# Kernel tuning notes

Hardware: AMD Instinct MI355X
Metric: run time of the kernel (lower is better)

The kernel has to match this reference:

```python
import jax, jax.numpy as jnp
import numpy as np

E = 128        # embed_dim
D = 384        # d_model
H = 12         # nhead
HD = D // H    # head_dim = 32
E2 = 64        # embed_dim_2d
E1 = 64        # embed_dim_1d
FF = 512       # dim_feedforward
EPS = 1e-5
SCALE = 1.0 / np.sqrt(D)  # dp_attn_norm='d_model'


def layer_norm(x, g, b):
    m = jnp.mean(x, axis=-1, keepdims=True)
    v = jnp.mean(jnp.square(x - m), axis=-1, keepdims=True)
    return (x - m) * jax.lax.rsqrt(v + EPS) * g + b


def setup_inputs() -> dict:
    key = jax.random.key(0)
    ks = jax.random.split(key, 16)
    L, B = 512, 8
    std = 0.02
    return {
        "s": jax.random.normal(ks[0], (L, B, E), jnp.float32),
        "x": jax.random.normal(ks[1], (L, B, E1), jnp.float32),
        "p": jax.random.normal(ks[2], (B, L, L, E2), jnp.float32),
        "Wq": jax.random.normal(ks[3], (E, D), jnp.float32) * std,
        "Wk": jax.random.normal(ks[4], (E, D), jnp.float32) * std,
        "Wv": jax.random.normal(ks[5], (E, D), jnp.float32) * std,
        "Wo": jax.random.normal(ks[6], (D, E), jnp.float32) * std,
        "bo": jnp.zeros((E,), jnp.float32),
        "W2d": jax.random.normal(ks[7], (E2, H), jnp.float32) * std,
        "b2d": jnp.zeros((H,), jnp.float32),
        "W1": jax.random.normal(ks[8], (E + E1, FF), jnp.float32) * std,
        "b1": jnp.zeros((FF,), jnp.float32),
        "W2": jax.random.normal(ks[9], (FF, E), jnp.float32) * std,
        "b2": jnp.zeros((E,), jnp.float32),
        "g1": jnp.ones((E,), jnp.float32),
        "beta1": jnp.zeros((E,), jnp.float32),
        "g2": jnp.ones((E,), jnp.float32),
        "beta2": jnp.zeros((E,), jnp.float32),
    }


def reference(s, x, p, Wq, Wk, Wv, Wo, bo, W2d, b2d, W1, b1, W2, b2,
              g1, beta1, g2, beta2):
    L, B, _ = s.shape
    # --- attention with additive 2D pair bias ---
    # (L,B,E)@(E,D) -> (L,B,D) -> (B,H,L,HD); head split matches torch view(L, B*H, HD)
    def heads(t):
        return jnp.transpose(t.reshape(L, B, H, HD), (1, 2, 0, 3))
    q = heads(s @ Wq) * SCALE
    k = heads(s @ Wk)
    v = heads(s @ Wv)
    scores = jnp.einsum('bhid,bhjd->bhij', q, k)
    pbias = jnp.transpose(p @ W2d + b2d, (0, 3, 1, 2))  # (B,L,L,H) -> (B,H,L,L)
    attn = jax.nn.softmax(scores + pbias, axis=-1)
    o = jnp.einsum('bhij,bhjd->bhid', attn, v)           # (B,H,L,HD)
    o = jnp.transpose(o, (2, 0, 1, 3)).reshape(L, B, D)  # back to (L,B,D)
    s2 = o @ Wo + bo
    # --- residual + post-LN ---
    s = layer_norm(s + s2, g1, beta1)
    # --- FFN on [s, x] concat ---
    um_in = jnp.concatenate([s, x], axis=-1)             # (L,B,E+E1)
    h = jax.nn.relu(um_in @ W1 + b1)
    s2 = h @ W2 + b2
    return layer_norm(s + s2, g2, beta2)
```

## Files before the change

kernel.cpp:

```cpp
#include <hip/hip_runtime.h>
#include <cstdint>
#include <cstddef>

#define EPS 1e-5f

__device__ __forceinline__ float4 ld4(const float* p) { return *(const float4*)p; }
__device__ __forceinline__ void st4(float* p, float4 v) { *(float4*)p = v; }

template<bool RELU>
__launch_bounds__(256)
__global__ void gemm_bias_kernel(const float* __restrict__ A1,
                                 const float* __restrict__ A2, int K1,
                                 const float* __restrict__ W,
                                 const float* __restrict__ bias,
                                 float* __restrict__ out,
                                 int N, int K) {
    __shared__ float As[32 * 68];
    __shared__ float Bs[32 * 68];
    const int tid = threadIdx.x;
    const int bx = blockIdx.x, by = blockIdx.y;
    const int tx = tid & 15, ty = tid >> 4;

    float acc[4][4];
#pragma unroll
    for (int a = 0; a < 4; ++a)
#pragma unroll
        for (int b = 0; b < 4; ++b) acc[a][b] = 0.f;

    for (int k0 = 0; k0 < K; k0 += 32) {
        __syncthreads();
#pragma unroll
        for (int itr = 0; itr < 2; ++itr) {
            int idx = tid + itr * 256;
            int r = idx >> 3, c4 = idx & 7;
            int kk = k0 + c4 * 4;
            const float* src; int rl, kl;
            if (kk < K1) { src = A1; rl = K1; kl = kk; }
            else         { src = A2; rl = K - K1; kl = kk - K1; }
            float4 a = ld4(&src[(size_t)(bx * 64 + r) * rl + kl]);
            As[(c4 * 4 + 0) * 68 + r] = a.x;
            As[(c4 * 4 + 1) * 68 + r] = a.y;
            As[(c4 * 4 + 2) * 68 + r] = a.z;
            As[(c4 * 4 + 3) * 68 + r] = a.w;
            int kb = idx >> 4, n4 = (idx & 15) * 4;
            float4 bvv = ld4(&W[(size_t)(k0 + kb) * N + by * 64 + n4]);
            st4(&Bs[kb * 68 + n4], bvv);
        }
        __syncthreads();
#pragma unroll
        for (int kk2 = 0; kk2 < 32; ++kk2) {
            float4 av = ld4(&As[kk2 * 68 + ty * 4]);
            float4 bv = ld4(&Bs[kk2 * 68 + tx * 4]);
            acc[0][0] = fmaf(av.x, bv.x, acc[0][0]);
            acc[0][1] = fmaf(av.x, bv.y, acc[0][1]);
            acc[0][2] = fmaf(av.x, bv.z, acc[0][2]);
            acc[0][3] = fmaf(av.x, bv.w, acc[0][3]);
            acc[1][0] = fmaf(av.y, bv.x, acc[1][0]);
            acc[1][1] = fmaf(av.y, bv.y, acc[1][1]);
            acc[1][2] = fmaf(av.y, bv.z, acc[1][2]);
            acc[1][3] = fmaf(av.y, bv.w, acc[1][3]);
            acc[2][0] = fmaf(av.z, bv.x, acc[2][0]);
            acc[2][1] = fmaf(av.z, bv.y, acc[2][1]);
            acc[2][2] = fmaf(av.z, bv.z, acc[2][2]);
            acc[2][3] = fmaf(av.z, bv.w, acc[2][3]);
            acc[3][0] = fmaf(av.w, bv.x, acc[3][0]);
            acc[3][1] = fmaf(av.w, bv.y, acc[3][1]);
            acc[3][2] = fmaf(av.w, bv.z, acc[3][2]);
            acc[3][3] = fmaf(av.w, bv.w, acc[3][3]);
        }
    }
    float4 bb = {0.f, 0.f, 0.f, 0.f};
    if (bias) bb = ld4(&bias[by * 64 + tx * 4]);
#pragma unroll
    for (int mi = 0; mi < 4; ++mi) {
        float4 y;
        y.x = acc[mi][0] + bb.x;
        y.y = acc[mi][1] + bb.y;
        y.z = acc[mi][2] + bb.z;
        y.w = acc[mi][3] + bb.w;
        if (RELU) {
            y.x = fmaxf(y.x, 0.f); y.y = fmaxf(y.y, 0.f);
            y.z = fmaxf(y.z, 0.f); y.w = fmaxf(y.w, 0.f);
        }
        st4(&out[(size_t)(bx * 64 + ty * 4 + mi) * N + by * 64 + tx * 4], y);
    }
}

__launch_bounds__(256)
__global__ void attn_kernel(const float* __restrict__ q,
                            const float* __restrict__ k,
                            const float* __restrict__ v,
                            const float* __restrict__ p,
                            const float* __restrict__ w2d,
                            const float* __restrict__ b2d,
                            float* __restrict__ o) {
    __shared__ float q_s[8 * 388];
    __shared__ float k_s[16 * 388];
    __shared__ float v_s[16 * 388];
    __shared__ float e_s[128 * 13];
    __shared__ float l_s[8][12];

    const int tid = threadIdx.x;
    const int it = blockIdx.x;
    const int b  = blockIdx.y;
    const int i0 = it * 8;
    const float scale = 0.05103103630798288f;

    for (int idx = tid; idx < 8 * 96; idx += 256) {
        int r = idx / 96, c4 = (idx % 96) * 4;
        float4 t = ld4(&q[(size_t)((i0 + r) * 8 + b) * 384 + c4]);
        t.x *= scale; t.y *= scale; t.z *= scale; t.w *= scale;
        st4(&q_s[r * 388 + c4], t);
    }

    const int half = __builtin_amdgcn_readfirstlane((int)(tid >> 7));
    const int pair = tid & 127;
    const int pi = pair >> 4, pj = pair & 15;
    const int e0 = half * 32;
    const int d0 = half * 16;
    const int i_b = tid >> 5, l32 = tid & 31;
    const float* w2dh = w2d + e0 * 12;

    float l_part[12];
#pragma unroll
    for (int h = 0; h < 12; ++h) l_part[h] = 0.f;
    float4 oacc[3];
#pragma unroll
    for (int c = 0; c < 3; ++c) { oacc[c].x = 0.f; oacc[c].y = 0.f; oacc[c].z = 0.f; oacc[c].w = 0.f; }

    for (int t = 0; t < 32; ++t) {
        const int j0 = t * 16;
        __syncthreads();
        for (int idx = tid; idx < 16 * 96; idx += 256) {
            int r = idx / 96, c4 = (idx % 96) * 4;
            size_t grow = (size_t)((j0 + r) * 8 + b) * 384 + c4;
            st4(&k_s[r * 388 + c4], ld4(&k[grow]));
            st4(&v_s[r * 388 + c4], ld4(&v[grow]));
        }
        __syncthreads();

        const float* pp = p + (((size_t)b * 512 + (i0 + pi)) * 512 + (j0 + pj)) * 64 + e0;
        float4 pr[8];
#pragma unroll
        for (int c = 0; c < 8; ++c) pr[c] = ld4(pp + c * 4);
        float S[12];
#pragma unroll
        for (int h = 0; h < 12; ++h) S[h] = (half == 0) ? b2d[h] : 0.f;
        const float* prf = (const float*)pr;
#pragma unroll
        for (int e = 0; e < 32; ++e) {
            float pe = prf[e];
#pragma unroll
            for (int h = 0; h < 12; ++h) S[h] = fmaf(pe, w2dh[e * 12 + h], S[h]);
        }
#pragma unroll
        for (int h = 0; h < 12; ++h) {
            const float4* qr4 = (const float4*)&q_s[pi * 388 + h * 32 + d0];
            const float4* kr4 = (const float4*)&k_s[pj * 388 + h * 32 + d0];
            float a0 = 0.f;
#pragma unroll
            for (int dd = 0; dd < 4; ++dd) {
                float4 qa = qr4[dd], ka = kr4[dd];
                a0 = fmaf(qa.x, ka.x, a0); a0 = fmaf(qa.y, ka.y, a0);
                a0 = fmaf(qa.z, ka.z, a0); a0 = fmaf(qa.w, ka.w, a0);
            }
            S[h] += a0;
        }
        if (half == 0) {
#pragma unroll
            for (int h = 0; h < 12; ++h) e_s[pair * 13 + h] = S[h];
        }
        __syncthreads();
        if (half == 1) {
#pragma unroll
            for (int h = 0; h < 12; ++h) {
                float E = __expf(S[h] + e_s[pair * 13 + h]);
                e_s[pair * 13 + h] = E;
                l_part[h] += E;
            }
        }
        __syncthreads();

#pragma unroll
        for (int j = 0; j < 16; ++j) {
            const float* er = &e_s[(i_b * 16 + j) * 13];
#pragma unroll
            for (int c = 0; c < 3; ++c) {
                float prob = er[c * 4 + (l32 >> 3)];
                float4 v4 = ld4(&v_s[j * 388 + c * 128 + l32 * 4]);
                oacc[c].x = fmaf(prob, v4.x, oacc[c].x);
                oacc[c].y = fmaf(prob, v4.y, oacc[c].y);
                oacc[c].z = fmaf(prob, v4.z, oacc[c].z);
                oacc[c].w = fmaf(prob, v4.w, oacc[c].w);
            }
        }
    }

    if (half == 1) {
#pragma unroll
        for (int h = 0; h < 12; ++h) {
            float s0 = l_part[h];
            s0 += __shfl_xor(s0, 1);
            s0 += __shfl_xor(s0, 2);
            s0 += __shfl_xor(s0, 4);
            s0 += __shfl_xor(s0, 8);
            l_part[h] = s0;
        }
        int lane = tid & 63;
        int il = lane >> 4;
        int hh = lane & 15;
        int grp = (tid >> 6) & 1;
        int ig = grp * 4 + il;
#pragma unroll
        for (int h = 0; h < 12; ++h)
            if (hh == h) l_s[ig][h] = l_part[h];
    }
    __syncthreads();
#pragma unroll
    for (int c = 0; c < 3; ++c) {
        float inv = 1.0f / l_s[i_b][c * 4 + (l32 >> 3)];
        float4 y;
        y.x = oacc[c].x * inv; y.y = oacc[c].y * inv;
        y.z = oacc[c].z * inv; y.w = oacc[c].w * inv;
        st4(&o[(size_t)((i0 + i_b) * 8 + b) * 384 + c * 128 + l32 * 4], y);
    }
}

__launch_bounds__(256)
__global__ void ln_kernel(const float* __restrict__ resid,
                          const float* __restrict__ y,
                          const float* __restrict__ g,
                          const float* __restrict__ be,
                          float* __restrict__ out) {
    const int tid = threadIdx.x;
    const int row = blockIdx.x * 2 + (tid >> 7);
    const int c = tid & 127;
    __shared__ float red[4][2];
    size_t idx = (size_t)row * 128 + c;
    float val = resid[idx] + y[idx];
    float s0 = val, sq = val * val;
#pragma unroll
    for (int m = 1; m <= 32; m <<= 1) {
        s0 += __shfl_xor(s0, m);
        sq += __shfl_xor(sq, m);
    }
    const int w = tid >> 6;
    if ((tid & 63) == 0) { red[w][0] = s0; red[w][1] = sq; }
    __syncthreads();
    float S  = red[w][0] + red[w ^ 1][0];
    float SQ = red[w][1] + red[w ^ 1][1];
    float mean = S * (1.f / 128.f);
    float var  = SQ * (1.f / 128.f) - mean * mean;
    out[idx] = (val - mean) * rsqrtf(var + EPS) * g[c] + be[c];
}

extern "C" void kernel_launch(void* const* d_in, const int* in_sizes, int n_in,
                              void* d_out, int out_size, void* d_ws, size_t ws_size,
                              hipStream_t stream) {
    const float* s   = (const float*)d_in[0];
    const float* x   = (const float*)d_in[1];
    const float* p   = (const float*)d_in[2];
    const float* Wq  = (const float*)d_in[3];
    const float* Wk  = (const float*)d_in[4];
    const float* Wv  = (const float*)d_in[5];
    const float* Wo  = (const float*)d_in[6];
    const float* bo  = (const float*)d_in[7];
    const float* W2d = (const float*)d_in[8];
    const float* b2d = (const float*)d_in[9];
    const float* W1  = (const float*)d_in[10];
    const float* b1  = (const float*)d_in[11];
    const float* W2  = (const float*)d_in[12];
    const float* b2  = (const float*)d_in[13];
    const float* g1  = (const float*)d_in[14];
    const float* be1 = (const float*)d_in[15];
    const float* g2  = (const float*)d_in[16];
    const float* be2 = (const float*)d_in[17];
    float* out = (float*)d_out;

    float* ws   = (float*)d_ws;
    float* q_ws = ws;
    float* k_ws = q_ws + 4096 * 384;
    float* v_ws = k_ws + 4096 * 384;
    float* o_ws = v_ws + 4096 * 384;
    float* t1   = o_ws + 4096 * 384;
    float* s1   = t1 + 4096 * 128;
    float* h_ws = s1 + 4096 * 128;
    float* t2   = h_ws + 4096 * 512;

    dim3 blk(256);
    gemm_bias_kernel<false><<<dim3(64, 6), blk, 0, stream>>>(s, nullptr, 128, Wq, nullptr, q_ws, 384, 128);
    gemm_bias_kernel<false><<<dim3(64, 6), blk, 0, stream>>>(s, nullptr, 128, Wk, nullptr, k_ws, 384, 128);
    gemm_bias_kernel<false><<<dim3(64, 6), blk, 0, stream>>>(s, nullptr, 128, Wv, nullptr, v_ws, 384, 128);
    attn_kernel<<<dim3(64, 8), blk, 0, stream>>>(q_ws, k_ws, v_ws, p, W2d, b2d, o_ws);
    gemm_bias_kernel<false><<<dim3(64, 2), blk, 0, stream>>>(o_ws, nullptr, 384, Wo, bo, t1, 128, 384);
    ln_kernel<<<dim3(2048), blk, 0, stream>>>(s, t1, g1, be1, s1);
    gemm_bias_kernel<true ><<<dim3(64, 8), blk, 0, stream>>>(s1, x, 128, W1, b1, h_ws, 512, 192);
    gemm_bias_kernel<false><<<dim3(64, 2), blk, 0, stream>>>(h_ws, nullptr, 512, W2, b2, t2, 128, 512);
    ln_kernel<<<dim3(2048), blk, 0, stream>>>(s1, t2, g2, be2, out);
}
```

Before: 1.048 ms.

## Split attention into MFMA scores and PV kernels with fp16 intermediates

Replaces the monolithic fp32 attention kernel with a scores kernel that computes the pair bias and QK^T via fp16 MFMA and writes exp'd scores to a full fp16 score matrix, plus a separate PV kernel using MFMA that normalizes by row sums. The QKV projections are fused into one launch that emits fp16 with the scale folded in, and the output-projection and FFN2 GEMMs are fused with residual add and LayerNorm. This removes scalar-FMA attention work and several launches, at the cost of writing and re-reading a large score buffer, reduced precision, and no max-subtraction in the softmax.

```diff
diff --git a/kernel.cpp b/kernel.cpp
--- a/kernel.cpp
+++ b/kernel.cpp
@@ -4,8 +4,273 @@
 
 #define EPS 1e-5f
 
+typedef _Float16 f16;
+typedef __attribute__((ext_vector_type(8))) _Float16 f16x8;
+typedef __attribute__((ext_vector_type(4))) _Float16 f16x4;
+typedef __attribute__((ext_vector_type(4))) float f32x4;
+
 __device__ __forceinline__ float4 ld4(const float* p) { return *(const float4*)p; }
 __device__ __forceinline__ void st4(float* p, float4 v) { *(float4*)p = v; }
+
+__launch_bounds__(256)
+__global__ void qkv_kernel(const float* __restrict__ A,
+                           const float* __restrict__ Wq,
+                           const float* __restrict__ Wk,
+                           const float* __restrict__ Wv,
+                           f16* __restrict__ qo, f16* __restrict__ ko,
+                           f16* __restrict__ vo) {
+    __shared__ float As[32 * 68];
+    __shared__ float Bs[32 * 68];
+    const int tid = threadIdx.x;
+    const int bx = blockIdx.x, by = blockIdx.y, z = blockIdx.z;
+    const float* Wp = (z == 0) ? Wq : ((z == 1) ? Wk : Wv);
+    f16* outp = (z == 0) ? qo : ((z == 1) ? ko : vo);
+    const float alpha = (z == 0) ? 0.05103103630798288f : 1.0f;
+    const int tx = tid & 15, ty = tid >> 4;
+    float acc[4][4] = {};
+    for (int k0 = 0; k0 < 128; k0 += 32) {
+        __syncthreads();
+#pragma unroll
+        for (int itr = 0; itr < 2; ++itr) {
+            int idx = tid + itr * 256;
+            int r = idx >> 3, c4 = idx & 7;
+            float4 a = ld4(&A[(size_t)(bx * 64 + r) * 128 + k0 + c4 * 4]);
+            As[(c4 * 4 + 0) * 68 + r] = a.x;
+            As[(c4 * 4 + 1) * 68 + r] = a.y;
+            As[(c4 * 4 + 2) * 68 + r] = a.z;
+            As[(c4 * 4 + 3) * 68 + r] = a.w;
+            int kb = idx >> 4, n4 = (idx & 15) * 4;
+            st4(&Bs[kb * 68 + n4], ld4(&Wp[(size_t)(k0 + kb) * 384 + by * 64 + n4]));
+        }
+        __syncthreads();
+#pragma unroll
+        for (int kk = 0; kk < 32; ++kk) {
+            float4 av = ld4(&As[kk * 68 + ty * 4]);
+            float4 bv = ld4(&Bs[kk * 68 + tx * 4]);
+            acc[0][0] = fmaf(av.x, bv.x, acc[0][0]);
+            acc[0][1] = fmaf(av.x, bv.y, acc[0][1]);
+            acc[0][2] = fmaf(av.x, bv.z, acc[0][2]);
+            acc[0][3] = fmaf(av.x, bv.w, acc[0][3]);
+            acc[1][0] = fmaf(av.y, bv.x, acc[1][0]);
+            acc[1][1] = fmaf(av.y, bv.y, acc[1][1]);
+            acc[1][2] = fmaf(av.y, bv.z, acc[1][2]);
+            acc[1][3] = fmaf(av.y, bv.w, acc[1][3]);
+            acc[2][0] = fmaf(av.z, bv.x, acc[2][0]);
+            acc[2][1] = fmaf(av.z, bv.y, acc[2][1]);
+            acc[2][2] = fmaf(av.z, bv.z, acc[2][2]);
+            acc[2][3] = fmaf(av.z, bv.w, acc[2][3]);
+            acc[3][0] = fmaf(av.w, bv.x, acc[3][0]);
+            acc[3][1] = fmaf(av.w, bv.y, acc[3][1]);
+            acc[3][2] = fmaf(av.w, bv.z, acc[3][2]);
+            acc[3][3] = fmaf(av.w, bv.w, acc[3][3]);
+        }
+    }
+#pragma unroll
+    for (int mi = 0; mi < 4; ++mi) {
+        f16x4 hv;
+        hv[0] = (f16)(acc[mi][0] * alpha);
+        hv[1] = (f16)(acc[mi][1] * alpha);
+        hv[2] = (f16)(acc[mi][2] * alpha);
+        hv[3] = (f16)(acc[mi][3] * alpha);
+        *(f16x4*)&outp[(size_t)(bx * 64 + ty * 4 + mi) * 384 + by * 64 + tx * 4] = hv;
+    }
+}
+
+__launch_bounds__(256)
+__global__ void scores_kernel(const f16* __restrict__ qw,
+                              const f16* __restrict__ kw,
+                              const float* __restrict__ p,
+                              const float* __restrict__ w2d,
+                              const float* __restrict__ b2d,
+                              f16* __restrict__ E) {
+    const int tid = threadIdx.x;
+    const int wv = tid >> 6, lane = tid & 63;
+    const int g = lane >> 4, lj = lane & 15;
+    const int jc = blockIdx.x, it = blockIdx.y, b = blockIdx.z;
+    const int i0 = it * 16, j0 = jc * 64 + wv * 16;
+
+    f16x8 qf[12];
+#pragma unroll
+    for (int h = 0; h < 12; ++h)
+        qf[h] = *(const f16x8*)&qw[((size_t)(i0 + lj) * 8 + b) * 384 + h * 32 + g * 8];
+
+    f32x4 acc[12];
+#pragma unroll
+    for (int h = 0; h < 12; ++h) {
+        float bb = b2d[h];
+        acc[h][0] = bb; acc[h][1] = bb; acc[h][2] = bb; acc[h][3] = bb;
+    }
+
+#pragma unroll
+    for (int r = 0; r < 4; ++r) {
+        const float* prow = p + (((size_t)b * 512 + i0 + g * 4 + r) * 512 + j0 + lj) * 64;
+#pragma unroll
+        for (int hf = 0; hf < 2; ++hf) {
+            float4 pb[8];
+#pragma unroll
+            for (int c = 0; c < 8; ++c) pb[c] = ld4(prow + hf * 32 + c * 4);
+            const float* pf = (const float*)pb;
+#pragma unroll
+            for (int e = 0; e < 32; ++e) {
+                float pe = pf[e];
+                const float* wrow = &w2d[(hf * 32 + e) * 12];
+#pragma unroll
+                for (int h = 0; h < 12; ++h) acc[h][r] = fmaf(pe, wrow[h], acc[h][r]);
+            }
+        }
+    }
+
+    f16x8 kf = *(const f16x8*)&kw[((size_t)(j0 + lj) * 8 + b) * 384 + g * 8];
+#pragma unroll
+    for (int h = 0; h < 12; ++h) {
+        f16x8 kn = kf;
+        if (h < 11)
+            kn = *(const f16x8*)&kw[((size_t)(j0 + lj) * 8 + b) * 384 + (h + 1) * 32 + g * 8];
+        acc[h] = __builtin_amdgcn_mfma_f32_16x16x32_f16(qf[h], kf, acc[h], 0, 0, 0);
+        kf = kn;
+    }
+
+#pragma unroll
+    for (int h = 0; h < 12; ++h) {
+        size_t ebase = (size_t)(b * 12 + h) * 512;
+#pragma unroll
+        for (int r = 0; r < 4; ++r) {
+            E[(ebase + i0 + g * 4 + r) * 512 + j0 + lj] = (f16)__expf(acc[h][r]);
+        }
+    }
+}
+
+__launch_bounds__(256)
+__global__ void pv_kernel(const f16* __restrict__ E,
+                          const f16* __restrict__ vw,
+                          float* __restrict__ o) {
+    __shared__ f16 vt[32][520];
+    const int tid = threadIdx.x;
+    const int bh = blockIdx.x;
+    const int b = bh / 12, h = bh % 12;
+    const int wv = tid >> 6, lane = tid & 63;
+    const int g = lane >> 4, lj = lane & 15;
+    const int i0 = blockIdx.y * 64 + wv * 16;
+
+#pragma unroll
+    for (int itr = 0; itr < 8; ++itr) {
+        int jl = itr * 64 + (tid >> 2);
+        int dc = (tid & 3) * 8;
+        f16x8 sv = *(const f16x8*)&vw[((size_t)jl * 8 + b) * 384 + h * 32 + dc];
+#pragma unroll
+        for (int dd = 0; dd < 8; ++dd) vt[dc + dd][jl] = sv[dd];
+    }
+    __syncthreads();
+
+    f32x4 acc0 = {}, acc1 = {};
+    float lsum = 0.f;
+    const f16* Erow = &E[((size_t)bh * 512 + i0 + lj) * 512];
+#pragma unroll
+    for (int ks = 0; ks < 16; ++ks) {
+        f16x8 af = *(const f16x8*)&Erow[ks * 32 + g * 8];
+        f16x8 b0 = *(const f16x8*)&vt[lj][ks * 32 + g * 8];
+        f16x8 b1 = *(const f16x8*)&vt[16 + lj][ks * 32 + g * 8];
+        acc0 = __builtin_amdgcn_mfma_f32_16x16x32_f16(af, b0, acc0, 0, 0, 0);
+        acc1 = __builtin_amdgcn_mfma_f32_16x16x32_f16(af, b1, acc1, 0, 0, 0);
+#pragma unroll
+        for (int d = 0; d < 8; ++d) lsum += (float)af[d];
+    }
+    lsum += __shfl_xor(lsum, 16);
+    lsum += __shfl_xor(lsum, 32);
+
+#pragma unroll
+    for (int r = 0; r < 4; ++r) {
+        float lr = __shfl(lsum, g * 4 + r);
+        float inv = 1.0f / lr;
+        size_t orow = ((size_t)(i0 + g * 4 + r) * 8 + b) * 384 + h * 32;
+        o[orow + lj] = acc0[r] * inv;
+        o[orow + 16 + lj] = acc1[r] * inv;
+    }
+}
+
+__launch_bounds__(256)
+__global__ void gemm_ln_kernel(const float* __restrict__ A, int K,
+                               const float* __restrict__ Wm,
+                               const float* __restrict__ bias,
+                               const float* __restrict__ resid,
+                               const float* __restrict__ gam,
+                               const float* __restrict__ bet,
+                               float* __restrict__ out) {
+    __shared__ float As[32][36];
+    __shared__ float Bs[32][132];
+    const int tid = threadIdx.x;
+    const int bx = blockIdx.x;
+    const int tx = tid & 31, ty = tid >> 5;
+    float acc[4][4] = {};
+    for (int k0 = 0; k0 < K; k0 += 32) {
+        __syncthreads();
+        {
+            int r = tid >> 3, c4 = tid & 7;
+            float4 a = ld4(&A[(size_t)(bx * 32 + r) * K + k0 + c4 * 4]);
+            As[c4 * 4 + 0][r] = a.x;
+            As[c4 * 4 + 1][r] = a.y;
+            As[c4 * 4 + 2][r] = a.z;
+            As[c4 * 4 + 3][r] = a.w;
+#pragma unroll
+            for (int itr = 0; itr < 4; ++itr) {
+                int idx = tid + itr * 256;
+                int kb = idx >> 5, n4 = (idx & 31) * 4;
+                st4(&Bs[kb][n4], ld4(&Wm[(size_t)(k0 + kb) * 128 + n4]));
+            }
+        }
+        __syncthreads();
+#pragma unroll
+        for (int kk = 0; kk < 32; ++kk) {
+            float4 av = ld4(&As[kk][ty * 4]);
+            float4 bv = ld4(&Bs[kk][tx * 4]);
+            acc[0][0] = fmaf(av.x, bv.x, acc[0][0]);
+            acc[0][1] = fmaf(av.x, bv.y, acc[0][1]);
+            acc[0][2] = fmaf(av.x, bv.z, acc[0][2]);
+            acc[0][3] = fmaf(av.x, bv.w, acc[0][3]);
+            acc[1][0] = fmaf(av.y, bv.x, acc[1][0]);
+            acc[1][1] = fmaf(av.y, bv.y, acc[1][1]);
+            acc[1][2] = fmaf(av.y, bv.z, acc[1][2]);
+            acc[1][3] = fmaf(av.y, bv.w, acc[1][3]);
+            acc[2][0] = fmaf(av.z, bv.x, acc[2][0]);
+            acc[2][1] = fmaf(av.z, bv.y, acc[2][1]);
+            acc[2][2] = fmaf(av.z, bv.z, acc[2][2]);
+            acc[2][3] = fmaf(av.z, bv.w, acc[2][3]);
+            acc[3][0] = fmaf(av.w, bv.x, acc[3][0]);
+            acc[3][1] = fmaf(av.w, bv.y, acc[3][1]);
+            acc[3][2] = fmaf(av.w, bv.z, acc[3][2]);
+            acc[3][3] = fmaf(av.w, bv.w, acc[3][3]);
+        }
+    }
+    float4 bb = ld4(&bias[tx * 4]);
+    float4 gg = ld4(&gam[tx * 4]);
+    float4 be4 = ld4(&bet[tx * 4]);
+#pragma unroll
+    for (int mi = 0; mi < 4; ++mi) {
+        int row = bx * 32 + ty * 4 + mi;
+        float4 r4 = ld4(&resid[(size_t)row * 128 + tx * 4]);
+        float4 y;
+        y.x = acc[mi][0] + bb.x + r4.x;
+        y.y = acc[mi][1] + bb.y + r4.y;
+        y.z = acc[mi][2] + bb.z + r4.z;
+        y.w = acc[mi][3] + bb.w + r4.w;
+        float s = y.x + y.y + y.z + y.w;
+        float sq = y.x * y.x + y.y * y.y + y.z * y.z + y.w * y.w;
+#pragma unroll
+        for (int m = 1; m <= 16; m <<= 1) {
+            s += __shfl_xor(s, m);
+            sq += __shfl_xor(sq, m);
+        }
+        float mean = s * (1.f / 128.f);
+        float var = sq * (1.f / 128.f) - mean * mean;
+        float rs = rsqrtf(var + EPS);
+        float4 w;
+        w.x = (y.x - mean) * rs * gg.x + be4.x;
+        w.y = (y.y - mean) * rs * gg.y + be4.y;
+        w.z = (y.z - mean) * rs * gg.z + be4.z;
+        w.w = (y.w - mean) * rs * gg.w + be4.w;
+        st4(&out[(size_t)row * 128 + tx * 4], w);
+    }
+}
 
 template<bool RELU>
 __launch_bounds__(256)
@@ -20,13 +285,7 @@
     const int tid = threadIdx.x;
     const int bx = blockIdx.x, by = blockIdx.y;
     const int tx = tid & 15, ty = tid >> 4;
-
-    float acc[4][4];
-#pragma unroll
-    for (int a = 0; a < 4; ++a)
-#pragma unroll
-        for (int b = 0; b < 4; ++b) acc[a][b] = 0.f;
-
+    float acc[4][4] = {};
     for (int k0 = 0; k0 < K; k0 += 32) {
         __syncthreads();
 #pragma unroll
@@ -43,8 +302,7 @@
             As[(c4 * 4 + 2) * 68 + r] = a.z;
             As[(c4 * 4 + 3) * 68 + r] = a.w;
             int kb = idx >> 4, n4 = (idx & 15) * 4;
-            float4 bvv = ld4(&W[(size_t)(k0 + kb) * N + by * 64 + n4]);
-            st4(&Bs[kb * 68 + n4], bvv);
+            st4(&Bs[kb * 68 + n4], ld4(&W[(size_t)(k0 + kb) * N + by * 64 + n4]));
         }
         __syncthreads();
 #pragma unroll
@@ -84,174 +342,6 @@
         }
         st4(&out[(size_t)(bx * 64 + ty * 4 + mi) * N + by * 64 + tx * 4], y);
     }
-}
-
-__launch_bounds__(256)
-__global__ void attn_kernel(const float* __restrict__ q,
-                            const float* __restrict__ k,
-                            const float* __restrict__ v,
-                            const float* __restrict__ p,
-                            const float* __restrict__ w2d,
-                            const float* __restrict__ b2d,
-                            float* __restrict__ o) {
-    __shared__ float q_s[8 * 388];
-    __shared__ float k_s[16 * 388];
-    __shared__ float v_s[16 * 388];
-    __shared__ float e_s[128 * 13];
-    __shared__ float l_s[8][12];
-
-    const int tid = threadIdx.x;
-    const int it = blockIdx.x;
-    const int b  = blockIdx.y;
-    const int i0 = it * 8;
-    const float scale = 0.05103103630798288f;
-
-    for (int idx = tid; idx < 8 * 96; idx += 256) {
-        int r = idx / 96, c4 = (idx % 96) * 4;
-        float4 t = ld4(&q[(size_t)((i0 + r) * 8 + b) * 384 + c4]);
-        t.x *= scale; t.y *= scale; t.z *= scale; t.w *= scale;
-        st4(&q_s[r * 388 + c4], t);
-    }
-
-    const int half = __builtin_amdgcn_readfirstlane((int)(tid >> 7));
-    const int pair = tid & 127;
-    const int pi = pair >> 4, pj = pair & 15;
-    const int e0 = half * 32;
-    const int d0 = half * 16;
-    const int i_b = tid >> 5, l32 = tid & 31;
-    const float* w2dh = w2d + e0 * 12;
-
-    float l_part[12];
-#pragma unroll
-    for (int h = 0; h < 12; ++h) l_part[h] = 0.f;
-    float4 oacc[3];
-#pragma unroll
-    for (int c = 0; c < 3; ++c) { oacc[c].x = 0.f; oacc[c].y = 0.f; oacc[c].z = 0.f; oacc[c].w = 0.f; }
-
-    for (int t = 0; t < 32; ++t) {
-        const int j0 = t * 16;
-        __syncthreads();
-        for (int idx = tid; idx < 16 * 96; idx += 256) {
-            int r = idx / 96, c4 = (idx % 96) * 4;
-            size_t grow = (size_t)((j0 + r) * 8 + b) * 384 + c4;
-            st4(&k_s[r * 388 + c4], ld4(&k[grow]));
-            st4(&v_s[r * 388 + c4], ld4(&v[grow]));
-        }
-        __syncthreads();
-
-        const float* pp = p + (((size_t)b * 512 + (i0 + pi)) * 512 + (j0 + pj)) * 64 + e0;
-        float4 pr[8];
-#pragma unroll
-        for (int c = 0; c < 8; ++c) pr[c] = ld4(pp + c * 4);
-        float S[12];
-#pragma unroll
-        for (int h = 0; h < 12; ++h) S[h] = (half == 0) ? b2d[h] : 0.f;
-        const float* prf = (const float*)pr;
-#pragma unroll
-        for (int e = 0; e < 32; ++e) {
-            float pe = prf[e];
-#pragma unroll
-            for (int h = 0; h < 12; ++h) S[h] = fmaf(pe, w2dh[e * 12 + h], S[h]);
-        }
-#pragma unroll
-        for (int h = 0; h < 12; ++h) {
-            const float4* qr4 = (const float4*)&q_s[pi * 388 + h * 32 + d0];
-            const float4* kr4 = (const float4*)&k_s[pj * 388 + h * 32 + d0];
-            float a0 = 0.f;
-#pragma unroll
-            for (int dd = 0; dd < 4; ++dd) {
-                float4 qa = qr4[dd], ka = kr4[dd];
-                a0 = fmaf(qa.x, ka.x, a0); a0 = fmaf(qa.y, ka.y, a0);
-                a0 = fmaf(qa.z, ka.z, a0); a0 = fmaf(qa.w, ka.w, a0);
-            }
-            S[h] += a0;
-        }
-        if (half == 0) {
-#pragma unroll
-            for (int h = 0; h < 12; ++h) e_s[pair * 13 + h] = S[h];
-        }
-        __syncthreads();
-        if (half == 1) {
-#pragma unroll
-            for (int h = 0; h < 12; ++h) {
-                float E = __expf(S[h] + e_s[pair * 13 + h]);
-                e_s[pair * 13 + h] = E;
-                l_part[h] += E;
-            }
-        }
-        __syncthreads();
-
-#pragma unroll
-        for (int j = 0; j < 16; ++j) {
-            const float* er = &e_s[(i_b * 16 + j) * 13];
-#pragma unroll
-            for (int c = 0; c < 3; ++c) {
-                float prob = er[c * 4 + (l32 >> 3)];
-                float4 v4 = ld4(&v_s[j * 388 + c * 128 + l32 * 4]);
-                oacc[c].x = fmaf(prob, v4.x, oacc[c].x);
-                oacc[c].y = fmaf(prob, v4.y, oacc[c].y);
-                oacc[c].z = fmaf(prob, v4.z, oacc[c].z);
-                oacc[c].w = fmaf(prob, v4.w, oacc[c].w);
-            }
-        }
-    }
-
-    if (half == 1) {
-#pragma unroll
-        for (int h = 0; h < 12; ++h) {
-            float s0 = l_part[h];
-            s0 += __shfl_xor(s0, 1);
-            s0 += __shfl_xor(s0, 2);
-            s0 += __shfl_xor(s0, 4);
-            s0 += __shfl_xor(s0, 8);
-            l_part[h] = s0;
-        }
-        int lane = tid & 63;
-        int il = lane >> 4;
-        int hh = lane & 15;
-        int grp = (tid >> 6) & 1;
-        int ig = grp * 4 + il;
-#pragma unroll
-        for (int h = 0; h < 12; ++h)
-            if (hh == h) l_s[ig][h] = l_part[h];
-    }
-    __syncthreads();
-#pragma unroll
-    for (int c = 0; c < 3; ++c) {
-        float inv = 1.0f / l_s[i_b][c * 4 + (l32 >> 3)];
-        float4 y;
-        y.x = oacc[c].x * inv; y.y = oacc[c].y * inv;
-        y.z = oacc[c].z * inv; y.w = oacc[c].w * inv;
-        st4(&o[(size_t)((i0 + i_b) * 8 + b) * 384 + c * 128 + l32 * 4], y);
-    }
-}
-
-__launch_bounds__(256)
-__global__ void ln_kernel(const float* __restrict__ resid,
-                          const float* __restrict__ y,
-                          const float* __restrict__ g,
-                          const float* __restrict__ be,
-                          float* __restrict__ out) {
-    const int tid = threadIdx.x;
-    const int row = blockIdx.x * 2 + (tid >> 7);
-    const int c = tid & 127;
-    __shared__ float red[4][2];
-    size_t idx = (size_t)row * 128 + c;
-    float val = resid[idx] + y[idx];
-    float s0 = val, sq = val * val;
-#pragma unroll
-    for (int m = 1; m <= 32; m <<= 1) {
-        s0 += __shfl_xor(s0, m);
-        sq += __shfl_xor(sq, m);
-    }
-    const int w = tid >> 6;
-    if ((tid & 63) == 0) { red[w][0] = s0; red[w][1] = sq; }
-    __syncthreads();
-    float S  = red[w][0] + red[w ^ 1][0];
-    float SQ = red[w][1] + red[w ^ 1][1];
-    float mean = S * (1.f / 128.f);
-    float var  = SQ * (1.f / 128.f) - mean * mean;
-    out[idx] = (val - mean) * rsqrtf(var + EPS) * g[c] + be[c];
 }
 
 extern "C" void kernel_launch(void* const* d_in, const int* in_sizes, int n_in,
@@ -277,24 +367,20 @@
     const float* be2 = (const float*)d_in[17];
     float* out = (float*)d_out;
 
-    float* ws   = (float*)d_ws;
-    float* q_ws = ws;
-    float* k_ws = q_ws + 4096 * 384;
-    float* v_ws = k_ws + 4096 * 384;
-    float* o_ws = v_ws + 4096 * 384;
-    float* t1   = o_ws + 4096 * 384;
-    float* s1   = t1 + 4096 * 128;
+    char* W = (char*)d_ws;
+    f16* q_ws = (f16*)W;
+    f16* k_ws = q_ws + 4096 * 384;
+    f16* v_ws = (f16*)(W + 6291456);
+    f16* E_ws = (f16*)(W + 9437184);
+    float* o_ws = (float*)W;
+    float* s1   = (float*)(W + 9437184 + 50331648);
     float* h_ws = s1 + 4096 * 128;
-    float* t2   = h_ws + 4096 * 512;
 
     dim3 blk(256);
-    gemm_bias_kernel<false><<<dim3(64, 6), blk, 0, stream>>>(s, nullptr, 128, Wq, nullptr, q_ws, 384, 128);
-    gemm_bias_kernel<false><<<dim3(64, 6), blk, 0, stream>>>(s, nullptr, 128, Wk, nullptr, k_ws, 384, 128);
-    gemm_bias_kernel<false><<<dim3(64, 6), blk, 0, stream>>>(s, nullptr, 128, Wv, nullptr, v_ws, 384, 128);
-    attn_kernel<<<dim3(64, 8), blk, 0, stream>>>(q_ws, k_ws, v_ws, p, W2d, b2d, o_ws);
-    gemm_bias_kernel<false><<<dim3(64, 2), blk, 0, stream>>>(o_ws, nullptr, 384, Wo, bo, t1, 128, 384);
-    ln_kernel<<<dim3(2048), blk, 0, stream>>>(s, t1, g1, be1, s1);
-    gemm_bias_kernel<true ><<<dim3(64, 8), blk, 0, stream>>>(s1, x, 128, W1, b1, h_ws, 512, 192);
-    gemm_bias_kernel<false><<<dim3(64, 2), blk, 0, stream>>>(h_ws, nullptr, 512, W2, b2, t2, 128, 512);
-    ln_kernel<<<dim3(2048), blk, 0, stream>>>(s1, t2, g2, be2, out);
-}
+    qkv_kernel<<<dim3(64, 6, 3), blk, 0, stream>>>(s, Wq, Wk, Wv, q_ws, k_ws, v_ws);
+    scores_kernel<<<dim3(8, 32, 8), blk, 0, stream>>>(q_ws, k_ws, p, W2d, b2d, E_ws);
+    pv_kernel<<<dim3(96, 8), blk, 0, stream>>>(E_ws, v_ws, o_ws);
+    gemm_ln_kernel<<<dim3(128), blk, 0, stream>>>(o_ws, 384, Wo, bo, s, g1, be1, s1);
+    gemm_bias_kernel<true><<<dim3(64, 8), blk, 0, stream>>>(s1, x, 128, W1, b1, h_ws, 512, 192);
+    gemm_ln_kernel<<<dim3(128), blk, 0, stream>>>(h_ws, 512, W2, b2, s1, g2, be2, out);
+}
```

Result: no change. 1.061 ms (+1.3%).
